# Kernel optimization log

Hardware: AMD Instinct MI355X
Metric: run time of the kernel (lower is better)

The kernel has to match this reference:

```python
import jax, jax.numpy as jnp
import numpy as np

B, S, D, H = 2, 2048, 1024, 16
HD = D // H
FF = 4 * D
EPS = 1e-5


def _layernorm(x, g, b):
    m = jnp.mean(x, axis=-1, keepdims=True)
    v = jnp.var(x, axis=-1, keepdims=True)
    return (x - m) * jax.lax.rsqrt(v + EPS) * g + b


def setup_inputs() -> dict:
    key = jax.random.key(0)
    ks = jax.random.split(key, 13)
    s = lambda fan_in: 1.0 / np.sqrt(fan_in)
    return {
        "x": jax.random.normal(ks[0], (B, S, D), jnp.float32),
        "ln1_g": jnp.ones((D,), jnp.float32),
        "ln1_b": jnp.zeros((D,), jnp.float32),
        "w_qkv": jax.random.uniform(ks[1], (D, 3 * D), jnp.float32, -s(D), s(D)),
        "b_qkv": jax.random.uniform(ks[2], (3 * D,), jnp.float32, -s(D), s(D)),
        "w_proj": jax.random.uniform(ks[3], (D, D), jnp.float32, -s(D), s(D)),
        "b_proj": jax.random.uniform(ks[4], (D,), jnp.float32, -s(D), s(D)),
        "ln2_g": jnp.ones((D,), jnp.float32),
        "ln2_b": jnp.zeros((D,), jnp.float32),
        "w_fc1": jax.random.uniform(ks[5], (D, FF), jnp.float32, -s(D), s(D)),
        "b_fc1": jax.random.uniform(ks[6], (FF,), jnp.float32, -s(D), s(D)),
        "w_fc2": jax.random.uniform(ks[7], (FF, D), jnp.float32, -s(FF), s(FF)),
        "b_fc2": jax.random.uniform(ks[8], (D,), jnp.float32, -s(FF), s(FF)),
    }


def reference(x, ln1_g, ln1_b, w_qkv, b_qkv, w_proj, b_proj,
              ln2_g, ln2_b, w_fc1, b_fc1, w_fc2, b_fc2):
    scale = 1.0 / np.sqrt(HD)
    # pre-LN attention
    h = _layernorm(x, ln1_g, ln1_b)
    qkv = h @ w_qkv + b_qkv                                # [B,S,3D]
    qkv = qkv.reshape(B, S, 3, H, HD).transpose(2, 0, 3, 1, 4)
    q, k, v = qkv[0], qkv[1], qkv[2]                       # [B,H,S,HD]
    scores = jnp.einsum("bhqd,bhkd->bhqk", q, k) * scale   # [B,H,S,S]
    causal = jnp.tril(jnp.ones((S, S), bool))
    scores = jnp.where(causal, scores, -jnp.inf)
    attn = jax.nn.softmax(scores, axis=-1)
    out = jnp.einsum("bhqk,bhkd->bhqd", attn, v)           # [B,H,S,HD]
    out = out.transpose(0, 2, 1, 3).reshape(B, S, D)
    out = out @ w_proj + b_proj
    x = x + out
    # pre-LN MLP
    h = _layernorm(x, ln2_g, ln2_b)
    h = jax.nn.gelu(h @ w_fc1 + b_fc1, approximate=False)
    h = h @ w_fc2 + b_fc2
    return x + h
```

## Files before the change

### kernel.cpp

```cpp
#include <hip/hip_runtime.h>
#include <hip/hip_bf16.h>

#define BDIM 1024
#define SEQ  2048
#define NB   2
#define NH   16
#define HDIM 64
#define FFDIM 4096
#define MROWS (NB*SEQ)

typedef __attribute__((ext_vector_type(8))) short short8;
typedef __attribute__((ext_vector_type(4))) float f32x4;

static __device__ __forceinline__ unsigned short f2bf(float f) {
  union { float f; unsigned u; } v; v.f = f;
  unsigned r = v.u + 0x7fffu + ((v.u >> 16) & 1u);
  return (unsigned short)(r >> 16);
}

static __device__ __forceinline__ f32x4 splat4(float x) {
  f32x4 v; v[0] = x; v[1] = x; v[2] = x; v[3] = x; return v;
}

#define GLOAD16(gp, lp)                                                        \
  __builtin_amdgcn_global_load_lds(                                            \
      (const __attribute__((address_space(1))) void*)(gp),                     \
      (__attribute__((address_space(3))) void*)(lp), 16, 0, 0)

__global__ void tcvt_all(const float* __restrict__ w0, const float* __restrict__ w1,
                         const float* __restrict__ w2, const float* __restrict__ w3,
                         unsigned short* __restrict__ o0, unsigned short* __restrict__ o1,
                         unsigned short* __restrict__ o2, unsigned short* __restrict__ o3) {
  const int bid = blockIdx.x;
  const float* in; unsigned short* out; int R, C, nbx, rem;
  if (bid < 3072)      { in = w0; out = o0; R = 1024; C = 3072; rem = bid;        nbx = 96;  }
  else if (bid < 4096) { in = w1; out = o1; R = 1024; C = 1024; rem = bid - 3072; nbx = 32;  }
  else if (bid < 8192) { in = w2; out = o2; R = 1024; C = 4096; rem = bid - 4096; nbx = 128; }
  else                 { in = w3; out = o3; R = 4096; C = 1024; rem = bid - 8192; nbx = 32;  }
  const int c0 = (rem % nbx) * 32, r0 = (rem / nbx) * 32;
  __shared__ float tile[32][33];
  const int tx = threadIdx.x & 31, ty = threadIdx.x >> 5;
#pragma unroll
  for (int i = 0; i < 32; i += 8)
    tile[ty + i][tx] = in[(size_t)(r0 + ty + i) * C + c0 + tx];
  __syncthreads();
#pragma unroll
  for (int i = 0; i < 32; i += 8)
    out[(size_t)(c0 + ty + i) * R + r0 + tx] = f2bf(tile[tx][ty + i]);
}

__global__ void vtr_kernel(const unsigned short* __restrict__ qkv,
                           unsigned short* __restrict__ vt) {
  __shared__ unsigned short tile[32][33];
  const int h = blockIdx.z & 15, b = blockIdx.z >> 4;
  const int s0 = blockIdx.y * 32, d0 = blockIdx.x * 32;
  const int tx = threadIdx.x & 31, ty = threadIdx.x >> 5;
  const unsigned short* src = qkv + (size_t)b * SEQ * 3072 + 2048 + h * HDIM;
#pragma unroll
  for (int i = 0; i < 32; i += 8)
    tile[ty + i][tx] = src[(size_t)(s0 + ty + i) * 3072 + d0 + tx];
  __syncthreads();
  unsigned short* dst = vt + (size_t)(b * NH + h) * HDIM * SEQ;
#pragma unroll
  for (int i = 0; i < 32; i += 8)
    dst[(size_t)(d0 + ty + i) * SEQ + s0 + tx] = tile[tx][ty + i];
}

__global__ void ln_kernel(const float* __restrict__ x, const float* __restrict__ g,
                          const float* __restrict__ b, unsigned short* __restrict__ out) {
  const int row = blockIdx.x;
  const int tid = threadIdx.x;
  const float4 v = ((const float4*)(x + (size_t)row * BDIM))[tid];
  float s  = v.x + v.y + v.z + v.w;
  float ss = v.x * v.x + v.y * v.y + v.z * v.z + v.w * v.w;
#pragma unroll
  for (int off = 32; off; off >>= 1) { s += __shfl_xor(s, off); ss += __shfl_xor(ss, off); }
  __shared__ float red[8];
  const int wave = tid >> 6;
  if ((tid & 63) == 0) { red[wave * 2] = s; red[wave * 2 + 1] = ss; }
  __syncthreads();
  s  = red[0] + red[2] + red[4] + red[6];
  ss = red[1] + red[3] + red[5] + red[7];
  const float mean = s * (1.0f / BDIM);
  const float inv  = rsqrtf(ss * (1.0f / BDIM) - mean * mean + 1e-5f);
  const float4 gg = ((const float4*)g)[tid];
  const float4 bb = ((const float4*)b)[tid];
  ushort4 o;
  o.x = f2bf((v.x - mean) * inv * gg.x + bb.x);
  o.y = f2bf((v.y - mean) * inv * gg.y + bb.y);
  o.z = f2bf((v.z - mean) * inv * gg.z + bb.z);
  o.w = f2bf((v.w - mean) * inv * gg.w + bb.w);
  ((ushort4*)(out + (size_t)row * BDIM))[tid] = o;
}

template <int EPI>
__global__ __launch_bounds__(256, 2)
void gemm_bt(const unsigned short* __restrict__ A, const unsigned short* __restrict__ Bt,
             const float* __restrict__ bias, const float* __restrict__ resid,
             void* __restrict__ outp, int M, int N, int K) {
  __shared__ unsigned short As[128 * 32];
  __shared__ unsigned short Bs[128 * 32];
  const int tid = threadIdx.x;
  const int n0 = blockIdx.x * 128, m0 = blockIdx.y * 128;
  const int lane = tid & 63, wave = tid >> 6;
  const int lr = lane & 15, lg = lane >> 4;
  const int wr = (wave >> 1) * 64, wc = (wave & 1) * 64;

  const unsigned short* ga0 = A  + (size_t)(m0 + (tid >> 2)) * K + (tid & 3) * 8;
  const unsigned short* ga1 = ga0 + (size_t)64 * K;
  const unsigned short* gb0 = Bt + (size_t)(n0 + (tid >> 2)) * K + (tid & 3) * 8;
  const unsigned short* gb1 = gb0 + (size_t)64 * K;
  unsigned short* la0 = As + tid * 8;
  unsigned short* la1 = As + (256 + tid) * 8;
  unsigned short* lb0 = Bs + tid * 8;
  unsigned short* lb1 = Bs + (256 + tid) * 8;

  f32x4 acc[4][4];
#pragma unroll
  for (int i = 0; i < 4; i++)
#pragma unroll
    for (int j = 0; j < 4; j++) acc[i][j] = splat4(0.0f);

  for (int k0 = 0; k0 < K; k0 += 32) {
    GLOAD16(ga0 + k0, la0);
    GLOAD16(ga1 + k0, la1);
    GLOAD16(gb0 + k0, lb0);
    GLOAD16(gb1 + k0, lb1);
    __syncthreads();
    short8 af[4], bfr[4];
#pragma unroll
    for (int mi = 0; mi < 4; mi++)
      af[mi] = *(const short8*)(As + (wr + mi * 16 + lr) * 32 + lg * 8);
#pragma unroll
    for (int ni = 0; ni < 4; ni++)
      bfr[ni] = *(const short8*)(Bs + (wc + ni * 16 + lr) * 32 + lg * 8);
#pragma unroll
    for (int mi = 0; mi < 4; mi++)
#pragma unroll
      for (int ni = 0; ni < 4; ni++)
        acc[mi][ni] = __builtin_amdgcn_mfma_f32_16x16x32_bf16(af[mi], bfr[ni], acc[mi][ni], 0, 0, 0);
    __syncthreads();
  }

  float bv[4];
#pragma unroll
  for (int ni = 0; ni < 4; ni++) bv[ni] = bias[n0 + wc + ni * 16 + lr];
#pragma unroll
  for (int mi = 0; mi < 4; mi++) {
#pragma unroll
    for (int ni = 0; ni < 4; ni++) {
      const int row0 = m0 + wr + mi * 16 + lg * 4;
      const int col  = n0 + wc + ni * 16 + lr;
#pragma unroll
      for (int r = 0; r < 4; r++) {
        const float v = acc[mi][ni][r] + bv[ni];
        const size_t idx = (size_t)(row0 + r) * N + col;
        if constexpr (EPI == 0) {
          ((unsigned short*)outp)[idx] = f2bf(v);
        } else if constexpr (EPI == 1) {
          ((float*)outp)[idx] = v + resid[idx];
        } else {
          const float t = 0.5f * v * (1.0f + erff(v * 0.70710678118f));
          ((unsigned short*)outp)[idx] = f2bf(t);
        }
      }
    }
  }
}

__global__ __launch_bounds__(256, 3)
void attn_kernel(const unsigned short* __restrict__ qkv,
                 const unsigned short* __restrict__ vT,
                 unsigned short* __restrict__ out) {
  __shared__ unsigned short Ks[64 * 64];
  __shared__ unsigned short Vs[64 * 64];
  __shared__ unsigned short Ps[4][32 * 72];
  const int tid = threadIdx.x;
  const int wave = tid >> 6, lane = tid & 63;
  const int lr = lane & 15, lg = lane >> 4;
  const int Q0 = blockIdx.x * 128;
  const int wq0 = Q0 + wave * 32;
  const int h = blockIdx.y, bb = blockIdx.z;
  const size_t base = (size_t)bb * SEQ * 3072;
  const unsigned short* vth = vT + (size_t)(bb * NH + h) * HDIM * SEQ;
  unsigned short* psw = Ps[wave];
  const int sw = lr & 7;

  short8 qf[2][2];
#pragma unroll
  for (int qb = 0; qb < 2; ++qb)
#pragma unroll
    for (int kc = 0; kc < 2; ++kc)
      qf[qb][kc] = *(const short8*)(qkv + base +
          (size_t)(wq0 + qb * 16 + lr) * 3072 + h * HDIM + kc * 32 + lg * 8);

  f32x4 oacc[2][4];
#pragma unroll
  for (int qb = 0; qb < 2; ++qb)
#pragma unroll
    for (int n = 0; n < 4; ++n) oacc[qb][n] = splat4(0.0f);
  f32x4 m_i[2] = { splat4(-INFINITY), splat4(-INFINITY) };
  f32x4 l_i[2] = { splat4(0.0f), splat4(0.0f) };

  const int srow = tid >> 3;
  const int scb  = (tid & 7) ^ (srow & 7);
  const unsigned short* kg0 = qkv + base + (size_t)srow * 3072 + 1024 + h * HDIM + scb * 8;
  const unsigned short* vg0 = vth + (size_t)srow * SEQ + scb * 8;
  unsigned short* kl0 = Ks + tid * 8;
  unsigned short* kl1 = Ks + 2048 + tid * 8;
  unsigned short* vl0 = Vs + tid * 8;
  unsigned short* vl1 = Vs + 2048 + tid * 8;

  const int TB = Q0 / 64 + 2;

  for (int t = 0; t < TB; ++t) {
    const int kk = t * 64;
    __syncthreads();
    GLOAD16(kg0 + (size_t)kk * 3072, kl0);
    GLOAD16(kg0 + (size_t)(kk + 32) * 3072, kl1);
    GLOAD16(vg0 + kk, vl0);
    GLOAD16(vg0 + (size_t)32 * SEQ + kk, vl1);
    __syncthreads();

    short8 kf[4][2];
#pragma unroll
    for (int kb = 0; kb < 4; ++kb)
#pragma unroll
      for (int kc = 0; kc < 2; ++kc)
        kf[kb][kc] = *(const short8*)(Ks + (kb * 16 + lr) * 64 +
                                      (((kc * 4 + lg) ^ sw) * 8));
    f32x4 s[2][4];
#pragma unroll
    for (int qb = 0; qb < 2; ++qb)
#pragma unroll
      for (int kb = 0; kb < 4; ++kb) s[qb][kb] = splat4(0.0f);
    __builtin_amdgcn_s_setprio(1);
#pragma unroll
    for (int qb = 0; qb < 2; ++qb)
#pragma unroll
      for (int kb = 0; kb < 4; ++kb) {
        s[qb][kb] = __builtin_amdgcn_mfma_f32_16x16x32_bf16(qf[qb][0], kf[kb][0], s[qb][kb], 0, 0, 0);
        s[qb][kb] = __builtin_amdgcn_mfma_f32_16x16x32_bf16(qf[qb][1], kf[kb][1], s[qb][kb], 0, 0, 0);
      }
    __builtin_amdgcn_s_setprio(0);

    const bool nm = (kk + 64 > wq0);
#pragma unroll
    for (int qb = 0; qb < 2; ++qb)
#pragma unroll
      for (int kb = 0; kb < 4; ++kb)
#pragma unroll
        for (int r = 0; r < 4; ++r) {
          float v = s[qb][kb][r] * 0.125f;
          if (nm) {
            const int q = wq0 + qb * 16 + lg * 4 + r;
            if (kk + kb * 16 + lr > q) v = -INFINITY;
          }
          s[qb][kb][r] = v;
        }

    f32x4 mx[2];
#pragma unroll
    for (int qb = 0; qb < 2; ++qb) {
#pragma unroll
      for (int r = 0; r < 4; ++r)
        mx[qb][r] = fmaxf(fmaxf(s[qb][0][r], s[qb][1][r]),
                          fmaxf(s[qb][2][r], s[qb][3][r]));
    }
#pragma unroll
    for (int msk = 1; msk < 16; msk <<= 1)
#pragma unroll
      for (int qb = 0; qb < 2; ++qb)
#pragma unroll
        for (int r = 0; r < 4; ++r)
          mx[qb][r] = fmaxf(mx[qb][r], __shfl_xor(mx[qb][r], msk));
    f32x4 mnew[2], corr[2];
#pragma unroll
    for (int qb = 0; qb < 2; ++qb)
#pragma unroll
      for (int r = 0; r < 4; ++r) {
        mnew[qb][r] = fmaxf(m_i[qb][r], mx[qb][r]);
        corr[qb][r] = __expf(m_i[qb][r] - mnew[qb][r]);
      }
#pragma unroll
    for (int qb = 0; qb < 2; ++qb)
#pragma unroll
      for (int kb = 0; kb < 4; ++kb)
#pragma unroll
        for (int r = 0; r < 4; ++r)
          s[qb][kb][r] = __expf(s[qb][kb][r] - mnew[qb][r]);
    f32x4 ps[2];
#pragma unroll
    for (int qb = 0; qb < 2; ++qb)
#pragma unroll
      for (int r = 0; r < 4; ++r)
        ps[qb][r] = (s[qb][0][r] + s[qb][1][r]) + (s[qb][2][r] + s[qb][3][r]);
#pragma unroll
    for (int msk = 1; msk < 16; msk <<= 1)
#pragma unroll
      for (int qb = 0; qb < 2; ++qb)
#pragma unroll
        for (int r = 0; r < 4; ++r)
          ps[qb][r] += __shfl_xor(ps[qb][r], msk);
#pragma unroll
    for (int qb = 0; qb < 2; ++qb)
#pragma unroll
      for (int r = 0; r < 4; ++r) {
        l_i[qb][r] = l_i[qb][r] * corr[qb][r] + ps[qb][r];
        m_i[qb][r] = mnew[qb][r];
      }
#pragma unroll
    for (int qb = 0; qb < 2; ++qb)
#pragma unroll
      for (int n = 0; n < 4; ++n)
#pragma unroll
        for (int r = 0; r < 4; ++r) oacc[qb][n][r] *= corr[qb][r];

#pragma unroll
    for (int qb = 0; qb < 2; ++qb)
#pragma unroll
      for (int kb = 0; kb < 4; ++kb)
#pragma unroll
        for (int r = 0; r < 4; ++r)
          psw[(qb * 16 + lg * 4 + r) * 72 + kb * 16 + lr] = f2bf(s[qb][kb][r]);

    short8 pf[2][2], vf[4][2];
#pragma unroll
    for (int qb = 0; qb < 2; ++qb)
#pragma unroll
      for (int kc = 0; kc < 2; ++kc)
        pf[qb][kc] = *(const short8*)(psw + (qb * 16 + lr) * 72 + kc * 32 + lg * 8);
#pragma unroll
    for (int n = 0; n < 4; ++n)
#pragma unroll
      for (int kc = 0; kc < 2; ++kc)
        vf[n][kc] = *(const short8*)(Vs + (n * 16 + lr) * 64 +
                                     (((kc * 4 + lg) ^ sw) * 8));
    __builtin_amdgcn_s_setprio(1);
#pragma unroll
    for (int qb = 0; qb < 2; ++qb)
#pragma unroll
      for (int n = 0; n < 4; ++n) {
        oacc[qb][n] = __builtin_amdgcn_mfma_f32_16x16x32_bf16(pf[qb][0], vf[n][0], oacc[qb][n], 0, 0, 0);
        oacc[qb][n] = __builtin_amdgcn_mfma_f32_16x16x32_bf16(pf[qb][1], vf[n][1], oacc[qb][n], 0, 0, 0);
      }
    __builtin_amdgcn_s_setprio(0);
  }

  f32x4 linv[2];
#pragma unroll
  for (int qb = 0; qb < 2; ++qb)
#pragma unroll
    for (int r = 0; r < 4; ++r) linv[qb][r] = 1.0f / l_i[qb][r];
#pragma unroll
  for (int qb = 0; qb < 2; ++qb)
#pragma unroll
    for (int n = 0; n < 4; ++n)
#pragma unroll
      for (int r = 0; r < 4; ++r)
        out[(size_t)(bb * SEQ + wq0 + qb * 16 + lg * 4 + r) * BDIM + h * HDIM + n * 16 + lr]
            = f2bf(oacc[qb][n][r] * linv[qb][r]);
}

extern "C" void kernel_launch(void* const* d_in, const int* in_sizes, int n_in,
                              void* d_out, int out_size, void* d_ws, size_t ws_size,
                              hipStream_t stream) {
  const float* x      = (const float*)d_in[0];
  const float* ln1_g  = (const float*)d_in[1];
  const float* ln1_b  = (const float*)d_in[2];
  const float* w_qkv  = (const float*)d_in[3];
  const float* b_qkv  = (const float*)d_in[4];
  const float* w_proj = (const float*)d_in[5];
  const float* b_proj = (const float*)d_in[6];
  const float* ln2_g  = (const float*)d_in[7];
  const float* ln2_b  = (const float*)d_in[8];
  const float* w_fc1  = (const float*)d_in[9];
  const float* b_fc1  = (const float*)d_in[10];
  const float* w_fc2  = (const float*)d_in[11];
  const float* b_fc2  = (const float*)d_in[12];
  float* out = (float*)d_out;

  char* ws = (char*)d_ws;
  unsigned short* wqkvT  = (unsigned short*)(ws + 0);
  unsigned short* wprojT = (unsigned short*)(ws + 6291456);
  unsigned short* wfc1T  = (unsigned short*)(ws + 8388608);
  unsigned short* wfc2T  = (unsigned short*)(ws + 16777216);
  unsigned short* hbuf   = (unsigned short*)(ws + 25165824);
  float*          x2     = (float*)         (ws + 33554432);
  unsigned short* qkvb   = (unsigned short*)(ws + 50331648);
  unsigned short* attnb  = (unsigned short*)(ws + 75497472);
  unsigned short* fc1b   = (unsigned short*)(ws + 50331648);

  tcvt_all<<<12288, 256, 0, stream>>>(w_qkv, w_proj, w_fc1, w_fc2,
                                      wqkvT, wprojT, wfc1T, wfc2T);

  ln_kernel<<<MROWS, 256, 0, stream>>>(x, ln1_g, ln1_b, hbuf);
  gemm_bt<0><<<dim3(3072 / 128, MROWS / 128), 256, 0, stream>>>(hbuf, wqkvT, b_qkv, nullptr, qkvb, MROWS, 3072, 1024);
  vtr_kernel<<<dim3(HDIM / 32, SEQ / 32, NB * NH), 256, 0, stream>>>(qkvb, hbuf);
  attn_kernel<<<dim3(SEQ / 128, NH, NB), 256, 0, stream>>>(qkvb, hbuf, attnb);
  gemm_bt<1><<<dim3(1024 / 128, MROWS / 128), 256, 0, stream>>>(attnb, wprojT, b_proj, x, x2, MROWS, 1024, 1024);

  ln_kernel<<<MROWS, 256, 0, stream>>>(x2, ln2_g, ln2_b, hbuf);
  gemm_bt<2><<<dim3(4096 / 128, MROWS / 128), 256, 0, stream>>>(hbuf, wfc1T, b_fc1, nullptr, fc1b, MROWS, FFDIM, 1024);
  gemm_bt<1><<<dim3(1024 / 128, MROWS / 128), 256, 0, stream>>>(fc1b, wfc2T, b_fc2, x2, out, MROWS, 1024, FFDIM);
}
```

Baseline: 443.9 us.

## Shrink attention query tile and add 64-wide GEMM for N=1024 projections

The attention kernel now handles 64 query rows per block, with one 16-row tile per wave. This doubles the grid and removes the wasted extra key tile per block. Softmax uses exp2 with a prescaled log2e factor, and occupancy bounds are raised for attention and the generic GEMM. A new 128x64-tile GEMM serves the N=1024 proj and fc2 layers, giving twice as many blocks so the CUs fill better. In exchange, each block gets less data reuse, and the new GEMM reads the A tile twice as often.

```diff
diff --git a/kernel.cpp b/kernel.cpp
--- a/kernel.cpp
+++ b/kernel.cpp
@@ -94,7 +94,7 @@
 }
 
 template <int EPI>
-__global__ __launch_bounds__(256, 2)
+__global__ __launch_bounds__(256, 3)
 void gemm_bt(const unsigned short* __restrict__ A, const unsigned short* __restrict__ Bt,
              const float* __restrict__ bias, const float* __restrict__ resid,
              void* __restrict__ outp, int M, int N, int K) {
@@ -169,38 +169,98 @@
 }
 
 __global__ __launch_bounds__(256, 3)
+void gemm_bt_n64(const unsigned short* __restrict__ A, const unsigned short* __restrict__ Bt,
+                 const float* __restrict__ bias, const float* __restrict__ resid,
+                 float* __restrict__ outp, int M, int N, int K) {
+  __shared__ unsigned short As[128 * 32];
+  __shared__ unsigned short Bs[64 * 32];
+  const int tid = threadIdx.x;
+  const int n0 = blockIdx.x * 64, m0 = blockIdx.y * 128;
+  const int lane = tid & 63, wave = tid >> 6;
+  const int lr = lane & 15, lg = lane >> 4;
+  const int wr = wave * 32;
+
+  const unsigned short* ga0 = A  + (size_t)(m0 + (tid >> 2)) * K + (tid & 3) * 8;
+  const unsigned short* ga1 = ga0 + (size_t)64 * K;
+  const unsigned short* gb0 = Bt + (size_t)(n0 + (tid >> 2)) * K + (tid & 3) * 8;
+  unsigned short* la0 = As + tid * 8;
+  unsigned short* la1 = As + (256 + tid) * 8;
+  unsigned short* lb0 = Bs + tid * 8;
+
+  f32x4 acc[2][4];
+#pragma unroll
+  for (int i = 0; i < 2; i++)
+#pragma unroll
+    for (int j = 0; j < 4; j++) acc[i][j] = splat4(0.0f);
+
+  for (int k0 = 0; k0 < K; k0 += 32) {
+    GLOAD16(ga0 + k0, la0);
+    GLOAD16(ga1 + k0, la1);
+    GLOAD16(gb0 + k0, lb0);
+    __syncthreads();
+    short8 af[2], bfr[4];
+#pragma unroll
+    for (int mi = 0; mi < 2; mi++)
+      af[mi] = *(const short8*)(As + (wr + mi * 16 + lr) * 32 + lg * 8);
+#pragma unroll
+    for (int ni = 0; ni < 4; ni++)
+      bfr[ni] = *(const short8*)(Bs + (ni * 16 + lr) * 32 + lg * 8);
+#pragma unroll
+    for (int mi = 0; mi < 2; mi++)
+#pragma unroll
+      for (int ni = 0; ni < 4; ni++)
+        acc[mi][ni] = __builtin_amdgcn_mfma_f32_16x16x32_bf16(af[mi], bfr[ni], acc[mi][ni], 0, 0, 0);
+    __syncthreads();
+  }
+
+  float bv[4];
+#pragma unroll
+  for (int ni = 0; ni < 4; ni++) bv[ni] = bias[n0 + ni * 16 + lr];
+#pragma unroll
+  for (int mi = 0; mi < 2; mi++) {
+#pragma unroll
+    for (int ni = 0; ni < 4; ni++) {
+      const int row0 = m0 + wr + mi * 16 + lg * 4;
+      const int col  = n0 + ni * 16 + lr;
+#pragma unroll
+      for (int r = 0; r < 4; r++) {
+        const size_t idx = (size_t)(row0 + r) * N + col;
+        outp[idx] = acc[mi][ni][r] + bv[ni] + resid[idx];
+      }
+    }
+  }
+}
+
+__global__ __launch_bounds__(256, 4)
 void attn_kernel(const unsigned short* __restrict__ qkv,
                  const unsigned short* __restrict__ vT,
                  unsigned short* __restrict__ out) {
   __shared__ unsigned short Ks[64 * 64];
   __shared__ unsigned short Vs[64 * 64];
-  __shared__ unsigned short Ps[4][32 * 72];
+  __shared__ unsigned short Ps[4][16 * 72];
   const int tid = threadIdx.x;
   const int wave = tid >> 6, lane = tid & 63;
   const int lr = lane & 15, lg = lane >> 4;
-  const int Q0 = blockIdx.x * 128;
-  const int wq0 = Q0 + wave * 32;
+  const int Q0 = blockIdx.x * 64;
+  const int wq0 = Q0 + wave * 16;
   const int h = blockIdx.y, bb = blockIdx.z;
   const size_t base = (size_t)bb * SEQ * 3072;
   const unsigned short* vth = vT + (size_t)(bb * NH + h) * HDIM * SEQ;
   unsigned short* psw = Ps[wave];
   const int sw = lr & 7;
-
-  short8 qf[2][2];
-#pragma unroll
-  for (int qb = 0; qb < 2; ++qb)
-#pragma unroll
-    for (int kc = 0; kc < 2; ++kc)
-      qf[qb][kc] = *(const short8*)(qkv + base +
-          (size_t)(wq0 + qb * 16 + lr) * 3072 + h * HDIM + kc * 32 + lg * 8);
-
-  f32x4 oacc[2][4];
-#pragma unroll
-  for (int qb = 0; qb < 2; ++qb)
-#pragma unroll
-    for (int n = 0; n < 4; ++n) oacc[qb][n] = splat4(0.0f);
-  f32x4 m_i[2] = { splat4(-INFINITY), splat4(-INFINITY) };
-  f32x4 l_i[2] = { splat4(0.0f), splat4(0.0f) };
+  const float SC = 0.125f * 1.44269504089f;
+
+  short8 qf[2];
+#pragma unroll
+  for (int kc = 0; kc < 2; ++kc)
+    qf[kc] = *(const short8*)(qkv + base +
+        (size_t)(wq0 + lr) * 3072 + h * HDIM + kc * 32 + lg * 8);
+
+  f32x4 oacc[4];
+#pragma unroll
+  for (int n = 0; n < 4; ++n) oacc[n] = splat4(0.0f);
+  f32x4 m_i = splat4(-INFINITY);
+  f32x4 l_i = splat4(0.0f);
 
   const int srow = tid >> 3;
   const int scb  = (tid & 7) ^ (srow & 7);
@@ -211,7 +271,7 @@
   unsigned short* vl0 = Vs + tid * 8;
   unsigned short* vl1 = Vs + 2048 + tid * 8;
 
-  const int TB = Q0 / 64 + 2;
+  const int TB = blockIdx.x + 1;
 
   for (int t = 0; t < TB; ++t) {
     const int kk = t * 64;
@@ -229,107 +289,79 @@
       for (int kc = 0; kc < 2; ++kc)
         kf[kb][kc] = *(const short8*)(Ks + (kb * 16 + lr) * 64 +
                                       (((kc * 4 + lg) ^ sw) * 8));
-    f32x4 s[2][4];
-#pragma unroll
-    for (int qb = 0; qb < 2; ++qb)
-#pragma unroll
-      for (int kb = 0; kb < 4; ++kb) s[qb][kb] = splat4(0.0f);
+    f32x4 s[4];
+#pragma unroll
+    for (int kb = 0; kb < 4; ++kb) s[kb] = splat4(0.0f);
     __builtin_amdgcn_s_setprio(1);
 #pragma unroll
-    for (int qb = 0; qb < 2; ++qb)
-#pragma unroll
-      for (int kb = 0; kb < 4; ++kb) {
-        s[qb][kb] = __builtin_amdgcn_mfma_f32_16x16x32_bf16(qf[qb][0], kf[kb][0], s[qb][kb], 0, 0, 0);
-        s[qb][kb] = __builtin_amdgcn_mfma_f32_16x16x32_bf16(qf[qb][1], kf[kb][1], s[qb][kb], 0, 0, 0);
+    for (int kb = 0; kb < 4; ++kb) {
+      s[kb] = __builtin_amdgcn_mfma_f32_16x16x32_bf16(qf[0], kf[kb][0], s[kb], 0, 0, 0);
+      s[kb] = __builtin_amdgcn_mfma_f32_16x16x32_bf16(qf[1], kf[kb][1], s[kb], 0, 0, 0);
+    }
+    __builtin_amdgcn_s_setprio(0);
+
+    const bool nm = (kk + 64 > wq0);
+#pragma unroll
+    for (int kb = 0; kb < 4; ++kb)
+#pragma unroll
+      for (int r = 0; r < 4; ++r) {
+        float v = s[kb][r] * SC;
+        if (nm) {
+          const int q = wq0 + lg * 4 + r;
+          if (kk + kb * 16 + lr > q) v = -INFINITY;
+        }
+        s[kb][r] = v;
       }
-    __builtin_amdgcn_s_setprio(0);
-
-    const bool nm = (kk + 64 > wq0);
-#pragma unroll
-    for (int qb = 0; qb < 2; ++qb)
-#pragma unroll
-      for (int kb = 0; kb < 4; ++kb)
-#pragma unroll
-        for (int r = 0; r < 4; ++r) {
-          float v = s[qb][kb][r] * 0.125f;
-          if (nm) {
-            const int q = wq0 + qb * 16 + lg * 4 + r;
-            if (kk + kb * 16 + lr > q) v = -INFINITY;
-          }
-          s[qb][kb][r] = v;
-        }
-
-    f32x4 mx[2];
-#pragma unroll
-    for (int qb = 0; qb < 2; ++qb) {
+
+    f32x4 mx;
+#pragma unroll
+    for (int r = 0; r < 4; ++r)
+      mx[r] = fmaxf(fmaxf(s[0][r], s[1][r]), fmaxf(s[2][r], s[3][r]));
+#pragma unroll
+    for (int msk = 1; msk < 16; msk <<= 1)
 #pragma unroll
       for (int r = 0; r < 4; ++r)
-        mx[qb][r] = fmaxf(fmaxf(s[qb][0][r], s[qb][1][r]),
-                          fmaxf(s[qb][2][r], s[qb][3][r]));
-    }
+        mx[r] = fmaxf(mx[r], __shfl_xor(mx[r], msk));
+    f32x4 mnew, corr;
+#pragma unroll
+    for (int r = 0; r < 4; ++r) {
+      mnew[r] = fmaxf(m_i[r], mx[r]);
+      corr[r] = exp2f(m_i[r] - mnew[r]);
+    }
+#pragma unroll
+    for (int kb = 0; kb < 4; ++kb)
+#pragma unroll
+      for (int r = 0; r < 4; ++r)
+        s[kb][r] = exp2f(s[kb][r] - mnew[r]);
+    f32x4 ps;
+#pragma unroll
+    for (int r = 0; r < 4; ++r)
+      ps[r] = (s[0][r] + s[1][r]) + (s[2][r] + s[3][r]);
 #pragma unroll
     for (int msk = 1; msk < 16; msk <<= 1)
 #pragma unroll
-      for (int qb = 0; qb < 2; ++qb)
-#pragma unroll
-        for (int r = 0; r < 4; ++r)
-          mx[qb][r] = fmaxf(mx[qb][r], __shfl_xor(mx[qb][r], msk));
-    f32x4 mnew[2], corr[2];
-#pragma unroll
-    for (int qb = 0; qb < 2; ++qb)
-#pragma unroll
-      for (int r = 0; r < 4; ++r) {
-        mnew[qb][r] = fmaxf(m_i[qb][r], mx[qb][r]);
-        corr[qb][r] = __expf(m_i[qb][r] - mnew[qb][r]);
-      }
-#pragma unroll
-    for (int qb = 0; qb < 2; ++qb)
-#pragma unroll
-      for (int kb = 0; kb < 4; ++kb)
-#pragma unroll
-        for (int r = 0; r < 4; ++r)
-          s[qb][kb][r] = __expf(s[qb][kb][r] - mnew[qb][r]);
-    f32x4 ps[2];
-#pragma unroll
-    for (int qb = 0; qb < 2; ++qb)
-#pragma unroll
       for (int r = 0; r < 4; ++r)
-        ps[qb][r] = (s[qb][0][r] + s[qb][1][r]) + (s[qb][2][r] + s[qb][3][r]);
-#pragma unroll
-    for (int msk = 1; msk < 16; msk <<= 1)
-#pragma unroll
-      for (int qb = 0; qb < 2; ++qb)
-#pragma unroll
-        for (int r = 0; r < 4; ++r)
-          ps[qb][r] += __shfl_xor(ps[qb][r], msk);
-#pragma unroll
-    for (int qb = 0; qb < 2; ++qb)
-#pragma unroll
-      for (int r = 0; r < 4; ++r) {
-        l_i[qb][r] = l_i[qb][r] * corr[qb][r] + ps[qb][r];
-        m_i[qb][r] = mnew[qb][r];
-      }
-#pragma unroll
-    for (int qb = 0; qb < 2; ++qb)
-#pragma unroll
-      for (int n = 0; n < 4; ++n)
-#pragma unroll
-        for (int r = 0; r < 4; ++r) oacc[qb][n][r] *= corr[qb][r];
-
-#pragma unroll
-    for (int qb = 0; qb < 2; ++qb)
-#pragma unroll
-      for (int kb = 0; kb < 4; ++kb)
-#pragma unroll
-        for (int r = 0; r < 4; ++r)
-          psw[(qb * 16 + lg * 4 + r) * 72 + kb * 16 + lr] = f2bf(s[qb][kb][r]);
-
-    short8 pf[2][2], vf[4][2];
-#pragma unroll
-    for (int qb = 0; qb < 2; ++qb)
-#pragma unroll
-      for (int kc = 0; kc < 2; ++kc)
-        pf[qb][kc] = *(const short8*)(psw + (qb * 16 + lr) * 72 + kc * 32 + lg * 8);
+        ps[r] += __shfl_xor(ps[r], msk);
+#pragma unroll
+    for (int r = 0; r < 4; ++r) {
+      l_i[r] = l_i[r] * corr[r] + ps[r];
+      m_i[r] = mnew[r];
+    }
+#pragma unroll
+    for (int n = 0; n < 4; ++n)
+#pragma unroll
+      for (int r = 0; r < 4; ++r) oacc[n][r] *= corr[r];
+
+#pragma unroll
+    for (int kb = 0; kb < 4; ++kb)
+#pragma unroll
+      for (int r = 0; r < 4; ++r)
+        psw[(lg * 4 + r) * 72 + kb * 16 + lr] = f2bf(s[kb][r]);
+
+    short8 pf[2], vf[4][2];
+#pragma unroll
+    for (int kc = 0; kc < 2; ++kc)
+      pf[kc] = *(const short8*)(psw + lr * 72 + kc * 32 + lg * 8);
 #pragma unroll
     for (int n = 0; n < 4; ++n)
 #pragma unroll
@@ -338,28 +370,22 @@
                                      (((kc * 4 + lg) ^ sw) * 8));
     __builtin_amdgcn_s_setprio(1);
 #pragma unroll
-    for (int qb = 0; qb < 2; ++qb)
-#pragma unroll
-      for (int n = 0; n < 4; ++n) {
-        oacc[qb][n] = __builtin_amdgcn_mfma_f32_16x16x32_bf16(pf[qb][0], vf[n][0], oacc[qb][n], 0, 0, 0);
-        oacc[qb][n] = __builtin_amdgcn_mfma_f32_16x16x32_bf16(pf[qb][1], vf[n][1], oacc[qb][n], 0, 0, 0);
-      }
+    for (int n = 0; n < 4; ++n) {
+      oacc[n] = __builtin_amdgcn_mfma_f32_16x16x32_bf16(pf[0], vf[n][0], oacc[n], 0, 0, 0);
+      oacc[n] = __builtin_amdgcn_mfma_f32_16x16x32_bf16(pf[1], vf[n][1], oacc[n], 0, 0, 0);
+    }
     __builtin_amdgcn_s_setprio(0);
   }
 
-  f32x4 linv[2];
-#pragma unroll
-  for (int qb = 0; qb < 2; ++qb)
-#pragma unroll
-    for (int r = 0; r < 4; ++r) linv[qb][r] = 1.0f / l_i[qb][r];
-#pragma unroll
-  for (int qb = 0; qb < 2; ++qb)
-#pragma unroll
-    for (int n = 0; n < 4; ++n)
-#pragma unroll
-      for (int r = 0; r < 4; ++r)
-        out[(size_t)(bb * SEQ + wq0 + qb * 16 + lg * 4 + r) * BDIM + h * HDIM + n * 16 + lr]
-            = f2bf(oacc[qb][n][r] * linv[qb][r]);
+  f32x4 linv;
+#pragma unroll
+  for (int r = 0; r < 4; ++r) linv[r] = 1.0f / l_i[r];
+#pragma unroll
+  for (int n = 0; n < 4; ++n)
+#pragma unroll
+    for (int r = 0; r < 4; ++r)
+      out[(size_t)(bb * SEQ + wq0 + lg * 4 + r) * BDIM + h * HDIM + n * 16 + lr]
+          = f2bf(oacc[n][r] * linv[r]);
 }
 
 extern "C" void kernel_launch(void* const* d_in, const int* in_sizes, int n_in,
@@ -397,10 +423,10 @@
   ln_kernel<<<MROWS, 256, 0, stream>>>(x, ln1_g, ln1_b, hbuf);
   gemm_bt<0><<<dim3(3072 / 128, MROWS / 128), 256, 0, stream>>>(hbuf, wqkvT, b_qkv, nullptr, qkvb, MROWS, 3072, 1024);
   vtr_kernel<<<dim3(HDIM / 32, SEQ / 32, NB * NH), 256, 0, stream>>>(qkvb, hbuf);
-  attn_kernel<<<dim3(SEQ / 128, NH, NB), 256, 0, stream>>>(qkvb, hbuf, attnb);
-  gemm_bt<1><<<dim3(1024 / 128, MROWS / 128), 256, 0, stream>>>(attnb, wprojT, b_proj, x, x2, MROWS, 1024, 1024);
+  attn_kernel<<<dim3(SEQ / 64, NH, NB), 256, 0, stream>>>(qkvb, hbuf, attnb);
+  gemm_bt_n64<<<dim3(1024 / 64, MROWS / 128), 256, 0, stream>>>(attnb, wprojT, b_proj, x, x2, MROWS, 1024, 1024);
 
   ln_kernel<<<MROWS, 256, 0, stream>>>(x2, ln2_g, ln2_b, hbuf);
   gemm_bt<2><<<dim3(4096 / 128, MROWS / 128), 256, 0, stream>>>(hbuf, wfc1T, b_fc1, nullptr, fc1b, MROWS, FFDIM, 1024);
-  gemm_bt<1><<<dim3(1024 / 128, MROWS / 128), 256, 0, stream>>>(fc1b, wfc2T, b_fc2, x2, out, MROWS, 1024, FFDIM);
-}
+  gemm_bt_n64<<<dim3(1024 / 64, MROWS / 128), 256, 0, stream>>>(fc1b, wfc2T, b_fc2, x2, out, MROWS, 1024, FFDIM);
+}
```

After: 436.8 us. About the same (-1.6%).
